# Kernel tuning notes

Hardware: AMD Instinct MI355X
Metric: run time of the kernel (lower is better)

Reference implementation:

```python
import jax, jax.numpy as jnp
import numpy as np

DIM = 512
N_HEADS = 8
HEAD_DIM = DIM // N_HEADS
SCALE = HEAD_DIM ** -0.5
B, T = 2, 4096


def setup_inputs() -> dict:
    key = jax.random.key(0)
    k1, k2, k3, k4 = jax.random.split(key, 4)
    x = jax.random.normal(k1, (B, T, DIM), dtype=jnp.float32)
    mask = jnp.ones((T, T), dtype=jnp.int32)
    w_qkv = jax.random.normal(k2, (DIM, 3 * DIM), dtype=jnp.float32) * (DIM ** -0.5)
    w_out = jax.random.normal(k3, (DIM, DIM), dtype=jnp.float32) * (DIM ** -0.5)
    b_out = jax.random.normal(k4, (DIM,), dtype=jnp.float32) * 0.02
    return {"x": x, "mask": mask, "w_qkv": w_qkv, "w_out": w_out, "b_out": b_out}


def reference(x, mask, w_qkv, w_out, b_out):
    b, t, c = x.shape
    qkv = x @ w_qkv  # [b, t, 3c]
    q, k, v = jnp.split(qkv, 3, axis=-1)
    # [b, t, c] -> [b, h, t, hd]
    q = q.reshape(b, t, N_HEADS, HEAD_DIM).transpose(0, 2, 1, 3)
    k = k.reshape(b, t, N_HEADS, HEAD_DIM).transpose(0, 2, 1, 3)
    v = v.reshape(b, t, N_HEADS, HEAD_DIM).transpose(0, 2, 1, 3)
    scores = jnp.einsum('bhqd,bhkd->bhqk', q, k) * SCALE
    # dropout p=0.0 -> identity (applied pre-mask in original module)
    scores = jnp.where(mask == 0, jnp.float32(-jnp.inf), scores)
    p = jax.nn.softmax(scores, axis=-1)
    attn = jnp.einsum('bhqk,bhkd->bhqd', p, v)
    attn = attn.transpose(0, 2, 1, 3).reshape(b, t, c)
    return attn @ w_out.T + b_out
```

## Files before the change

kernel.cpp:

```cpp
#include <hip/hip_runtime.h>
#include <hip/hip_bf16.h>
#include <cstdint>
#include <cstddef>


typedef __bf16 bf16x8 __attribute__((ext_vector_type(8)));
typedef __bf16 bf16x4 __attribute__((ext_vector_type(4)));
typedef float  f32x4  __attribute__((ext_vector_type(4)));
typedef uint32_t u32x4 __attribute__((ext_vector_type(4)));

static constexpr int kBatch = 2;
static constexpr int kT     = 4096;
static constexpr int kDim   = 512;
static constexpr int kHD    = 64;
static constexpr int kM     = kBatch * kT;
static constexpr int kQKVN  = 3 * kDim;

#define LOG2E 1.4426950408889634f

#define GLDS16(gp, lp)                                                    \
    __builtin_amdgcn_global_load_lds(                                     \
        (const __attribute__((address_space(1))) void*)(gp),              \
        (__attribute__((address_space(3))) void*)(lp), 16, 0, 0)

__global__ __launch_bounds__(256) void prep_kernel(const float* __restrict__ x,
                                                   const float* __restrict__ w_out,
                                                   const float* __restrict__ w_qkv,
                                                   __bf16* __restrict__ xb,
                                                   __bf16* __restrict__ wob,
                                                   __bf16* __restrict__ wqkvT) {
    const int bid = blockIdx.x, tid = threadIdx.x;
    if (bid < 4352) {
        const float* src = (bid < 4096) ? x : w_out;
        __bf16* dst = (bid < 4096) ? xb : wob;
        int i = ((bid < 4096) ? bid : (bid - 4096)) * 256 + tid;
        float4 v = reinterpret_cast<const float4*>(src)[i];
        __bf16 h[4] = {(__bf16)v.x, (__bf16)v.y, (__bf16)v.z, (__bf16)v.w};
        uint2 u;
        __builtin_memcpy(&u, h, 8);
        reinterpret_cast<uint2*>(dst)[i] = u;
        return;
    }
    __shared__ float tile[64][65];
    const int tb = bid - 4352;
    const int n0 = (tb % 24) * 64, k0 = (tb / 24) * 64;
#pragma unroll
    for (int p = 0; p < 4; ++p) {
        int v = p * 256 + tid;
        int r = v >> 4, c = (v & 15) << 2;
        float4 f = *reinterpret_cast<const float4*>(w_qkv + (size_t)(k0 + r) * kQKVN + n0 + c);
        tile[r][c] = f.x; tile[r][c + 1] = f.y; tile[r][c + 2] = f.z; tile[r][c + 3] = f.w;
    }
    __syncthreads();
#pragma unroll
    for (int p = 0; p < 2; ++p) {
        int v = p * 256 + tid;
        int r = v >> 3, c = (v & 7) << 3;
        bf16x8 o;
#pragma unroll
        for (int i = 0; i < 8; ++i) o[i] = (__bf16)tile[c + i][r];
        *reinterpret_cast<bf16x8*>(wqkvT + (size_t)(n0 + r) * kDim + k0 + c) = o;
    }
}

__global__ __launch_bounds__(256) void gemm_qkv(const __bf16* __restrict__ A,
                                                const __bf16* __restrict__ BT,
                                                __bf16* __restrict__ qkv,
                                                __bf16* __restrict__ vT) {
    const int K = kDim, N = kQKVN;
    __shared__ __bf16 As[2][128 * 32];
    __shared__ __bf16 Bs[2][128 * 32];
    const int tid  = threadIdx.x;
    const int lane = tid & 63, wave = tid >> 6;
    const int quad = lane >> 4, l16 = lane & 15;
    const int wm = wave >> 1, wn = wave & 1;
    const int m0 = blockIdx.x * 128;
    const int n0 = blockIdx.y * 128;
    const bool vtile = (n0 >= 1024);

    const int r16 = lane >> 2, c4 = lane & 3;
    const int swz = ((c4 ^ (r16 & 3)) << 3);
    const __bf16* ag0 = A  + (size_t)(m0 + wave * 32 + r16) * K + swz;
    const __bf16* ag1 = ag0 + (size_t)16 * K;
    const __bf16* bg0 = BT + (size_t)(n0 + wave * 32 + r16) * K + swz;
    const __bf16* bg1 = bg0 + (size_t)16 * K;
    const int ldst = wave * 2048;
    const int fsw = ((quad ^ (l16 & 3)) << 4);

    f32x4 acc[4][4] = {};

    auto stage = [&](int buf) {
        GLDS16(ag0, (char*)As[buf] + ldst);
        GLDS16(ag1, (char*)As[buf] + ldst + 1024);
        GLDS16(bg0, (char*)Bs[buf] + ldst);
        GLDS16(bg1, (char*)Bs[buf] + ldst + 1024);
        ag0 += 32; ag1 += 32; bg0 += 32; bg1 += 32;
    };

    stage(0);
    for (int it = 0; it < 16; ++it) {
        __builtin_amdgcn_s_barrier();
        stage((it + 1) & 1);
        asm volatile("s_waitcnt vmcnt(4)" ::: "memory");
        __builtin_amdgcn_s_barrier();

        const char* ab = (const char*)As[it & 1];
        const char* bb = (const char*)Bs[it & 1];
        bf16x8 af[4], bfr[4];
#pragma unroll
        for (int i = 0; i < 4; ++i)
            af[i] = *reinterpret_cast<const bf16x8*>(ab + (wm * 64 + i * 16 + l16) * 64 + fsw);
#pragma unroll
        for (int j = 0; j < 4; ++j)
            bfr[j] = *reinterpret_cast<const bf16x8*>(bb + (wn * 64 + j * 16 + l16) * 64 + fsw);
        if (!vtile) {
#pragma unroll
            for (int i = 0; i < 4; ++i)
#pragma unroll
                for (int j = 0; j < 4; ++j)
                    acc[i][j] = __builtin_amdgcn_mfma_f32_16x16x32_bf16(bfr[j], af[i], acc[i][j], 0, 0, 0);
        } else {
#pragma unroll
            for (int i = 0; i < 4; ++i)
#pragma unroll
                for (int j = 0; j < 4; ++j)
                    acc[i][j] = __builtin_amdgcn_mfma_f32_16x16x32_bf16(af[i], bfr[j], acc[i][j], 0, 0, 0);
        }
    }

    if (!vtile) {
#pragma unroll
        for (int i = 0; i < 4; ++i) {
            size_t mm = (size_t)m0 + wm * 64 + i * 16 + l16;
#pragma unroll
            for (int j = 0; j < 4; ++j) {
                int nn = n0 + wn * 64 + j * 16 + quad * 4;
                float sc = (nn < kDim) ? (0.125f * LOG2E) : 1.0f;
                bf16x4 ov;
#pragma unroll
                for (int r = 0; r < 4; ++r) ov[r] = (__bf16)(acc[i][j][r] * sc);
                *reinterpret_cast<bf16x4*>(qkv + mm * N + nn) = ov;
            }
        }
    } else {
        const int b = m0 >> 12;
#pragma unroll
        for (int j = 0; j < 4; ++j) {
            int dall = n0 - 1024 + wn * 64 + j * 16 + l16;
#pragma unroll
            for (int i = 0; i < 4; ++i) {
                int t = (m0 & 4095) + wm * 64 + i * 16 + quad * 4;
                bf16x4 ov;
#pragma unroll
                for (int r = 0; r < 4; ++r) ov[r] = (__bf16)(acc[i][j][r]);
                *reinterpret_cast<bf16x4*>(vT + (size_t)(b * 512 + dall) * kT + t) = ov;
            }
        }
    }
}

__global__ __launch_bounds__(256) void gemm_out64(const __bf16* __restrict__ A,
                                                  const __bf16* __restrict__ BT,
                                                  float* __restrict__ C,
                                                  const float* __restrict__ bias) {
    const int K = kDim, N = kDim;
    __shared__ __bf16 As[2][128 * 32];
    __shared__ __bf16 Bs[2][64 * 32];
    const int tid  = threadIdx.x;
    const int lane = tid & 63, wave = tid >> 6;
    const int quad = lane >> 4, l16 = lane & 15;
    const int m0 = blockIdx.x * 128;
    const int n0 = blockIdx.y * 64;

    const int r16 = lane >> 2, c4 = lane & 3;
    const int swz = ((c4 ^ (r16 & 3)) << 3);
    const __bf16* ag0 = A + (size_t)(m0 + wave * 32 + r16) * K + swz;
    const __bf16* ag1 = ag0 + (size_t)16 * K;
    const __bf16* bg  = BT + (size_t)(n0 + wave * 16 + r16) * K + swz;
    const int fsw = ((quad ^ (l16 & 3)) << 4);

    f32x4 acc[2][4] = {};

    auto stage = [&](int buf) {
        GLDS16(ag0, (char*)As[buf] + wave * 2048);
        GLDS16(ag1, (char*)As[buf] + wave * 2048 + 1024);
        GLDS16(bg,  (char*)Bs[buf] + wave * 1024);
        ag0 += 32; ag1 += 32; bg += 32;
    };

    stage(0);
    for (int it = 0; it < 16; ++it) {
        __builtin_amdgcn_s_barrier();
        stage((it + 1) & 1);
        asm volatile("s_waitcnt vmcnt(3)" ::: "memory");
        __builtin_amdgcn_s_barrier();

        const char* ab = (const char*)As[it & 1];
        const char* bb = (const char*)Bs[it & 1];
        bf16x8 af[2], bfr[4];
#pragma unroll
        for (int i = 0; i < 2; ++i)
            af[i] = *reinterpret_cast<const bf16x8*>(ab + (wave * 32 + i * 16 + l16) * 64 + fsw);
#pragma unroll
        for (int j = 0; j < 4; ++j)
            bfr[j] = *reinterpret_cast<const bf16x8*>(bb + (j * 16 + l16) * 64 + fsw);
#pragma unroll
        for (int i = 0; i < 2; ++i)
#pragma unroll
            for (int j = 0; j < 4; ++j)
                acc[i][j] = __builtin_amdgcn_mfma_f32_16x16x32_bf16(bfr[j], af[i], acc[i][j], 0, 0, 0);
    }

#pragma unroll
    for (int i = 0; i < 2; ++i) {
        size_t mm = (size_t)m0 + wave * 32 + i * 16 + l16;
#pragma unroll
        for (int j = 0; j < 4; ++j) {
            int nn = n0 + j * 16 + quad * 4;
            float4 bv = *reinterpret_cast<const float4*>(bias + nn);
            float4 o;
            o.x = acc[i][j][0] + bv.x;
            o.y = acc[i][j][1] + bv.y;
            o.z = acc[i][j][2] + bv.z;
            o.w = acc[i][j][3] + bv.w;
            *reinterpret_cast<float4*>(C + mm * N + nn) = o;
        }
    }
}

__global__ __launch_bounds__(256, 2) void attn_kernel(const __bf16* __restrict__ qkv,
                                                      const __bf16* __restrict__ vT,
                                                      __bf16* __restrict__ out) {
    __shared__ char smem[65536];
    const int qt = blockIdx.x, bh = blockIdx.y;
    const int b = bh >> 3, h = bh & 7;
    const int tid = threadIdx.x;
    const int lane = tid & 63, wave = tid >> 6;
    const int quad = lane >> 4, l16 = lane & 15;
    const int m7 = l16 & 7;
    const int qw = wave & 1, kw = wave >> 1;

    bf16x8 bq[4][2];
#pragma unroll
    for (int sq = 0; sq < 4; ++sq) {
        const __bf16* qrow =
            qkv + (size_t)(b * kT + qt * 128 + qw * 64 + sq * 16 + l16) * kQKVN + h * kHD;
        bq[sq][0] = *reinterpret_cast<const bf16x8*>(qrow + quad * 8);
        bq[sq][1] = *reinterpret_cast<const bf16x8*>(qrow + 32 + quad * 8);
    }

    bf16x8 onesf;
#pragma unroll
    for (int i = 0; i < 8; ++i) onesf[i] = (__bf16)1.0f;

    const int r8 = lane >> 3, c8 = lane & 7;
    const int swz = ((c8 ^ r8) << 3);
    const __bf16* kg[2];
    const __bf16* vg[2];
#pragma unroll
    for (int i = 0; i < 2; ++i) {
        kg[i] = qkv + (size_t)(b * kT + wave * 16 + i * 8 + r8) * kQKVN + kDim + h * kHD + swz;
        vg[i] = vT + (size_t)(bh * kHD + wave * 16 + i * 8 + r8) * kT + swz;
    }

    const int rowb = l16 << 7;
    const int adr0 = rowb + (((quad)     ^ m7) << 4);
    const int adr1 = rowb + (((quad + 4) ^ m7) << 4);

    f32x4 oT[4][4] = {};
    f32x4 lacc[4] = {};

    auto stage = [&](int buf) {
#pragma unroll
        for (int i = 0; i < 2; ++i) {
            GLDS16(kg[i], smem + buf * 8192 + wave * 2048 + i * 1024);
            GLDS16(vg[i], smem + 32768 + buf * 8192 + wave * 2048 + i * 1024);
            kg[i] += (size_t)64 * kQKVN;
            vg[i] += 64;
        }
    };

    auto qswap = [](uint32_t& a, uint32_t& bq_) {
        asm("v_permlane32_swap_b32 %0, %1" : "+v"(a), "+v"(bq_));
        asm("v_permlane16_swap_b32 %0, %1" : "+v"(a), "+v"(bq_));
    };

    auto compute = [&](int slot) {
        const char* kb = smem + slot * 8192;
        const char* vb = smem + 32768 + slot * 8192;
        bf16x8 k0[4], k1[4];
#pragma unroll
        for (int t = 0; t < 4; ++t) {
            k0[t] = *reinterpret_cast<const bf16x8*>(kb + adr0 + t * 2048);
            k1[t] = *reinterpret_cast<const bf16x8*>(kb + adr1 + t * 2048);
        }
        bf16x8 v0[4], v1[4];
#pragma unroll
        for (int dt = 0; dt < 4; ++dt) {
            v0[dt] = *reinterpret_cast<const bf16x8*>(vb + adr0 + dt * 2048);
            v1[dt] = *reinterpret_cast<const bf16x8*>(vb + adr1 + dt * 2048);
        }
#pragma unroll
        for (int sq = 0; sq < 4; ++sq) {
            f32x4 s[4] = {};
#pragma unroll
            for (int t = 0; t < 4; ++t) {
                s[t] = __builtin_amdgcn_mfma_f32_16x16x32_bf16(k0[t], bq[sq][0], s[t], 0, 0, 0);
                s[t] = __builtin_amdgcn_mfma_f32_16x16x32_bf16(k1[t], bq[sq][1], s[t], 0, 0, 0);
            }
            uint32_t c[4][2];
#pragma unroll
            for (int t = 0; t < 4; ++t) {
                float e0 = __builtin_amdgcn_exp2f(s[t][0]);
                float e1 = __builtin_amdgcn_exp2f(s[t][1]);
                float e2 = __builtin_amdgcn_exp2f(s[t][2]);
                float e3 = __builtin_amdgcn_exp2f(s[t][3]);
                asm("v_cvt_pk_bf16_f32 %0, %1, %2" : "=v"(c[t][0]) : "v"(e0), "v"(e1));
                asm("v_cvt_pk_bf16_f32 %0, %1, %2" : "=v"(c[t][1]) : "v"(e2), "v"(e3));
            }
            uint32_t a0 = c[0][0], b0 = c[1][0]; qswap(a0, b0);
            uint32_t a1 = c[0][1], b1 = c[1][1]; qswap(a1, b1);
            uint32_t a2 = c[2][0], b2 = c[3][0]; qswap(a2, b2);
            uint32_t a3 = c[2][1], b3 = c[3][1]; qswap(a3, b3);
            bf16x8 p0 = __builtin_bit_cast(bf16x8, (u32x4){a0, a1, b0, b1});
            bf16x8 p1 = __builtin_bit_cast(bf16x8, (u32x4){a2, a3, b2, b3});
#pragma unroll
            for (int dt = 0; dt < 4; ++dt) {
                oT[sq][dt] = __builtin_amdgcn_mfma_f32_16x16x32_bf16(v0[dt], p0, oT[sq][dt], 0, 0, 0);
                oT[sq][dt] = __builtin_amdgcn_mfma_f32_16x16x32_bf16(v1[dt], p1, oT[sq][dt], 0, 0, 0);
            }
            lacc[sq] = __builtin_amdgcn_mfma_f32_16x16x32_bf16(onesf, p0, lacc[sq], 0, 0, 0);
            lacc[sq] = __builtin_amdgcn_mfma_f32_16x16x32_bf16(onesf, p1, lacc[sq], 0, 0, 0);
        }
    };

    stage(0);
    stage(1);

    for (int p = 0; p < 32; ++p) {
        __builtin_amdgcn_s_barrier();
        stage((2 * p + 2) & 3);
        stage((2 * p + 3) & 3);
        asm volatile("s_waitcnt vmcnt(8)" ::: "memory");
        __builtin_amdgcn_s_barrier();
        compute((2 * p + kw) & 3);
    }

    __syncthreads();
    if (kw == 1) {
        char* basep = smem + qw * 16384;
#pragma unroll
        for (int sq = 0; sq < 4; ++sq) {
#pragma unroll
            for (int dt = 0; dt < 4; ++dt)
                *reinterpret_cast<f32x4*>(basep + ((sq * 4 + dt) * 64 + lane) * 16) = oT[sq][dt];
            *reinterpret_cast<float*>(smem + 32768 + qw * 1024 + sq * 256 + l16 * 4) = lacc[sq][0];
        }
    }
    __syncthreads();
    if (kw == 0) {
        const char* basep = smem + qw * 16384;
#pragma unroll
        for (int sq = 0; sq < 4; ++sq) {
            float lpart = *reinterpret_cast<const float*>(smem + 32768 + qw * 1024 + sq * 256 + l16 * 4);
            float inv = 1.f / (lacc[sq][0] + lpart);
            __bf16* ob = out + (size_t)(b * kT + qt * 128 + qw * 64 + sq * 16 + l16) * kDim + h * kHD;
#pragma unroll
            for (int dt = 0; dt < 4; ++dt) {
                f32x4 part = *reinterpret_cast<const f32x4*>(basep + ((sq * 4 + dt) * 64 + lane) * 16);
                bf16x4 ov;
#pragma unroll
                for (int r = 0; r < 4; ++r) ov[r] = (__bf16)((oT[sq][dt][r] + part[r]) * inv);
                *reinterpret_cast<bf16x4*>(ob + dt * 16 + quad * 4) = ov;
            }
        }
    }
}

extern "C" void kernel_launch(void* const* d_in, const int* in_sizes, int n_in,
                              void* d_out, int out_size, void* d_ws, size_t ws_size,
                              hipStream_t stream) {
    const float* x     = (const float*)d_in[0];
    const float* w_qkv = (const float*)d_in[2];
    const float* w_out = (const float*)d_in[3];
    const float* b_out = (const float*)d_in[4];
    float* out = (float*)d_out;

    char* ws = (char*)d_ws;
    __bf16* xb    = (__bf16*)(ws + 0x0000000);
    __bf16* wqkvT = (__bf16*)(ws + 0x0800000);
    __bf16* wob   = (__bf16*)(ws + 0x0980000);
    __bf16* qkv   = (__bf16*)(ws + 0x0A00000);
    __bf16* vT    = (__bf16*)(ws + 0x2200000);
    __bf16* attnb = (__bf16*)(ws + 0x2A00000);

    prep_kernel<<<dim3(4544), dim3(256), 0, stream>>>(x, w_out, w_qkv, xb, wob, wqkvT);

    gemm_qkv<<<dim3(kM / 128, kQKVN / 128), dim3(256), 0, stream>>>(xb, wqkvT, qkv, vT);

    attn_kernel<<<dim3(kT / 128, 16), dim3(256), 0, stream>>>(qkv, vT, attnb);

    gemm_out64<<<dim3(kM / 128, kDim / 64), dim3(256), 0, stream>>>(attnb, wob, out, b_out);
}
```

Measured before the change: 222.8 us.

## Split attention work across eight waves per block instead of four

The attention kernel now launches 512 threads per block. Each wave handles 32 query rows and half of each 64-key chunk, where before it handled 64 query rows and a whole chunk on alternating slots. Loading is spread over 8 waves at one load each, and every wave computes both staged slots per iteration. Per-wave register use drops and latency hiding should improve, at the cost of more barrier participants, repeated V fragment loads, and launch bounds of 4 that may force register limits.

```diff
diff --git a/kernel.cpp b/kernel.cpp
--- a/kernel.cpp
+++ b/kernel.cpp
@@ -228,7 +228,7 @@
     }
 }
 
-__global__ __launch_bounds__(256, 2) void attn_kernel(const __bf16* __restrict__ qkv,
+__global__ __launch_bounds__(512, 4) void attn_kernel(const __bf16* __restrict__ qkv,
                                                       const __bf16* __restrict__ vT,
                                                       __bf16* __restrict__ out) {
     __shared__ char smem[65536];
@@ -238,15 +238,15 @@
     const int lane = tid & 63, wave = tid >> 6;
     const int quad = lane >> 4, l16 = lane & 15;
     const int m7 = l16 & 7;
-    const int qw = wave & 1, kw = wave >> 1;
-
-    bf16x8 bq[4][2];
-#pragma unroll
-    for (int sq = 0; sq < 4; ++sq) {
+    const int qp = wave & 3, kh = wave >> 2;
+
+    bf16x8 bq[2][2];
+#pragma unroll
+    for (int j = 0; j < 2; ++j) {
         const __bf16* qrow =
-            qkv + (size_t)(b * kT + qt * 128 + qw * 64 + sq * 16 + l16) * kQKVN + h * kHD;
-        bq[sq][0] = *reinterpret_cast<const bf16x8*>(qrow + quad * 8);
-        bq[sq][1] = *reinterpret_cast<const bf16x8*>(qrow + 32 + quad * 8);
+            qkv + (size_t)(b * kT + qt * 128 + (qp * 2 + j) * 16 + l16) * kQKVN + h * kHD;
+        bq[j][0] = *reinterpret_cast<const bf16x8*>(qrow + quad * 8);
+        bq[j][1] = *reinterpret_cast<const bf16x8*>(qrow + 32 + quad * 8);
     }
 
     bf16x8 onesf;
@@ -255,29 +255,23 @@
 
     const int r8 = lane >> 3, c8 = lane & 7;
     const int swz = ((c8 ^ r8) << 3);
-    const __bf16* kg[2];
-    const __bf16* vg[2];
-#pragma unroll
-    for (int i = 0; i < 2; ++i) {
-        kg[i] = qkv + (size_t)(b * kT + wave * 16 + i * 8 + r8) * kQKVN + kDim + h * kHD + swz;
-        vg[i] = vT + (size_t)(bh * kHD + wave * 16 + i * 8 + r8) * kT + swz;
-    }
+    const __bf16* kg = qkv + (size_t)(b * kT + wave * 8 + r8) * kQKVN + kDim + h * kHD + swz;
+    const __bf16* vg = vT + (size_t)(bh * kHD + wave * 8 + r8) * kT + swz;
 
     const int rowb = l16 << 7;
     const int adr0 = rowb + (((quad)     ^ m7) << 4);
     const int adr1 = rowb + (((quad + 4) ^ m7) << 4);
-
-    f32x4 oT[4][4] = {};
-    f32x4 lacc[4] = {};
+    const int tk   = kh * 2;
+    const int vadr = kh ? adr1 : adr0;
+
+    f32x4 oT[2][4] = {};
+    f32x4 lacc[2] = {};
 
     auto stage = [&](int buf) {
-#pragma unroll
-        for (int i = 0; i < 2; ++i) {
-            GLDS16(kg[i], smem + buf * 8192 + wave * 2048 + i * 1024);
-            GLDS16(vg[i], smem + 32768 + buf * 8192 + wave * 2048 + i * 1024);
-            kg[i] += (size_t)64 * kQKVN;
-            vg[i] += 64;
-        }
+        GLDS16(kg, smem + buf * 8192 + wave * 1024);
+        GLDS16(vg, smem + 32768 + buf * 8192 + wave * 1024);
+        kg += (size_t)64 * kQKVN;
+        vg += 64;
     };
 
     auto qswap = [](uint32_t& a, uint32_t& bq_) {
@@ -288,49 +282,41 @@
     auto compute = [&](int slot) {
         const char* kb = smem + slot * 8192;
         const char* vb = smem + 32768 + slot * 8192;
-        bf16x8 k0[4], k1[4];
-#pragma unroll
-        for (int t = 0; t < 4; ++t) {
-            k0[t] = *reinterpret_cast<const bf16x8*>(kb + adr0 + t * 2048);
-            k1[t] = *reinterpret_cast<const bf16x8*>(kb + adr1 + t * 2048);
-        }
-        bf16x8 v0[4], v1[4];
-#pragma unroll
-        for (int dt = 0; dt < 4; ++dt) {
-            v0[dt] = *reinterpret_cast<const bf16x8*>(vb + adr0 + dt * 2048);
-            v1[dt] = *reinterpret_cast<const bf16x8*>(vb + adr1 + dt * 2048);
-        }
-#pragma unroll
-        for (int sq = 0; sq < 4; ++sq) {
-            f32x4 s[4] = {};
-#pragma unroll
-            for (int t = 0; t < 4; ++t) {
-                s[t] = __builtin_amdgcn_mfma_f32_16x16x32_bf16(k0[t], bq[sq][0], s[t], 0, 0, 0);
-                s[t] = __builtin_amdgcn_mfma_f32_16x16x32_bf16(k1[t], bq[sq][1], s[t], 0, 0, 0);
-            }
-            uint32_t c[4][2];
-#pragma unroll
-            for (int t = 0; t < 4; ++t) {
-                float e0 = __builtin_amdgcn_exp2f(s[t][0]);
-                float e1 = __builtin_amdgcn_exp2f(s[t][1]);
-                float e2 = __builtin_amdgcn_exp2f(s[t][2]);
-                float e3 = __builtin_amdgcn_exp2f(s[t][3]);
-                asm("v_cvt_pk_bf16_f32 %0, %1, %2" : "=v"(c[t][0]) : "v"(e0), "v"(e1));
-                asm("v_cvt_pk_bf16_f32 %0, %1, %2" : "=v"(c[t][1]) : "v"(e2), "v"(e3));
+        bf16x8 k0[2], k1[2];
+#pragma unroll
+        for (int i = 0; i < 2; ++i) {
+            k0[i] = *reinterpret_cast<const bf16x8*>(kb + adr0 + (tk + i) * 2048);
+            k1[i] = *reinterpret_cast<const bf16x8*>(kb + adr1 + (tk + i) * 2048);
+        }
+        bf16x8 vf[4];
+#pragma unroll
+        for (int dt = 0; dt < 4; ++dt)
+            vf[dt] = *reinterpret_cast<const bf16x8*>(vb + vadr + dt * 2048);
+#pragma unroll
+        for (int j = 0; j < 2; ++j) {
+            f32x4 s[2] = {};
+#pragma unroll
+            for (int i = 0; i < 2; ++i) {
+                s[i] = __builtin_amdgcn_mfma_f32_16x16x32_bf16(k0[i], bq[j][0], s[i], 0, 0, 0);
+                s[i] = __builtin_amdgcn_mfma_f32_16x16x32_bf16(k1[i], bq[j][1], s[i], 0, 0, 0);
+            }
+            uint32_t c[2][2];
+#pragma unroll
+            for (int i = 0; i < 2; ++i) {
+                float e0 = __builtin_amdgcn_exp2f(s[i][0]);
+                float e1 = __builtin_amdgcn_exp2f(s[i][1]);
+                float e2 = __builtin_amdgcn_exp2f(s[i][2]);
+                float e3 = __builtin_amdgcn_exp2f(s[i][3]);
+                asm("v_cvt_pk_bf16_f32 %0, %1, %2" : "=v"(c[i][0]) : "v"(e0), "v"(e1));
+                asm("v_cvt_pk_bf16_f32 %0, %1, %2" : "=v"(c[i][1]) : "v"(e2), "v"(e3));
             }
             uint32_t a0 = c[0][0], b0 = c[1][0]; qswap(a0, b0);
             uint32_t a1 = c[0][1], b1 = c[1][1]; qswap(a1, b1);
-            uint32_t a2 = c[2][0], b2 = c[3][0]; qswap(a2, b2);
-            uint32_t a3 = c[2][1], b3 = c[3][1]; qswap(a3, b3);
-            bf16x8 p0 = __builtin_bit_cast(bf16x8, (u32x4){a0, a1, b0, b1});
-            bf16x8 p1 = __builtin_bit_cast(bf16x8, (u32x4){a2, a3, b2, b3});
-#pragma unroll
-            for (int dt = 0; dt < 4; ++dt) {
-                oT[sq][dt] = __builtin_amdgcn_mfma_f32_16x16x32_bf16(v0[dt], p0, oT[sq][dt], 0, 0, 0);
-                oT[sq][dt] = __builtin_amdgcn_mfma_f32_16x16x32_bf16(v1[dt], p1, oT[sq][dt], 0, 0, 0);
-            }
-            lacc[sq] = __builtin_amdgcn_mfma_f32_16x16x32_bf16(onesf, p0, lacc[sq], 0, 0, 0);
-            lacc[sq] = __builtin_amdgcn_mfma_f32_16x16x32_bf16(onesf, p1, lacc[sq], 0, 0, 0);
+            bf16x8 p = __builtin_bit_cast(bf16x8, (u32x4){a0, a1, b0, b1});
+#pragma unroll
+            for (int dt = 0; dt < 4; ++dt)
+                oT[j][dt] = __builtin_amdgcn_mfma_f32_16x16x32_bf16(vf[dt], p, oT[j][dt], 0, 0, 0);
+            lacc[j] = __builtin_amdgcn_mfma_f32_16x16x32_bf16(onesf, p, lacc[j], 0, 0, 0);
         }
     };
 
@@ -341,36 +327,37 @@
         __builtin_amdgcn_s_barrier();
         stage((2 * p + 2) & 3);
         stage((2 * p + 3) & 3);
-        asm volatile("s_waitcnt vmcnt(8)" ::: "memory");
-        __builtin_amdgcn_s_barrier();
-        compute((2 * p + kw) & 3);
+        asm volatile("s_waitcnt vmcnt(4)" ::: "memory");
+        __builtin_amdgcn_s_barrier();
+        compute((2 * p) & 3);
+        compute((2 * p + 1) & 3);
     }
 
     __syncthreads();
-    if (kw == 1) {
-        char* basep = smem + qw * 16384;
-#pragma unroll
-        for (int sq = 0; sq < 4; ++sq) {
+    if (kh == 1) {
+        char* basep = smem + qp * 8192;
+#pragma unroll
+        for (int j = 0; j < 2; ++j) {
 #pragma unroll
             for (int dt = 0; dt < 4; ++dt)
-                *reinterpret_cast<f32x4*>(basep + ((sq * 4 + dt) * 64 + lane) * 16) = oT[sq][dt];
-            *reinterpret_cast<float*>(smem + 32768 + qw * 1024 + sq * 256 + l16 * 4) = lacc[sq][0];
+                *reinterpret_cast<f32x4*>(basep + ((j * 4 + dt) * 64 + lane) * 16) = oT[j][dt];
+            *reinterpret_cast<float*>(smem + 32768 + qp * 128 + j * 64 + l16 * 4) = lacc[j][0];
         }
     }
     __syncthreads();
-    if (kw == 0) {
-        const char* basep = smem + qw * 16384;
-#pragma unroll
-        for (int sq = 0; sq < 4; ++sq) {
-            float lpart = *reinterpret_cast<const float*>(smem + 32768 + qw * 1024 + sq * 256 + l16 * 4);
-            float inv = 1.f / (lacc[sq][0] + lpart);
-            __bf16* ob = out + (size_t)(b * kT + qt * 128 + qw * 64 + sq * 16 + l16) * kDim + h * kHD;
+    if (kh == 0) {
+        const char* basep = smem + qp * 8192;
+#pragma unroll
+        for (int j = 0; j < 2; ++j) {
+            float lpart = *reinterpret_cast<const float*>(smem + 32768 + qp * 128 + j * 64 + l16 * 4);
+            float inv = 1.f / (lacc[j][0] + lpart);
+            __bf16* ob = out + (size_t)(b * kT + qt * 128 + (qp * 2 + j) * 16 + l16) * kDim + h * kHD;
 #pragma unroll
             for (int dt = 0; dt < 4; ++dt) {
-                f32x4 part = *reinterpret_cast<const f32x4*>(basep + ((sq * 4 + dt) * 64 + lane) * 16);
+                f32x4 part = *reinterpret_cast<const f32x4*>(basep + ((j * 4 + dt) * 64 + lane) * 16);
                 bf16x4 ov;
 #pragma unroll
-                for (int r = 0; r < 4; ++r) ov[r] = (__bf16)((oT[sq][dt][r] + part[r]) * inv);
+                for (int r = 0; r < 4; ++r) ov[r] = (__bf16)((oT[j][dt][r] + part[r]) * inv);
                 *reinterpret_cast<bf16x4*>(ob + dt * 16 + quad * 4) = ov;
             }
         }
@@ -398,7 +385,7 @@
 
     gemm_qkv<<<dim3(kM / 128, kQKVN / 128), dim3(256), 0, stream>>>(xb, wqkvT, qkv, vT);
 
-    attn_kernel<<<dim3(kT / 128, 16), dim3(256), 0, stream>>>(qkv, vT, attnb);
+    attn_kernel<<<dim3(kT / 128, 16), dim3(512), 0, stream>>>(qkv, vT, attnb);
 
     gemm_out64<<<dim3(kM / 128, kDim / 64), dim3(256), 0, stream>>>(attnb, wob, out, b_out);
 }
```

New measurement: 223.9 us. No clear change (+0.5%).
